# Kernel tuning notes

Measured on AMD Instinct MI355X. Metric: run time of the kernel, lower is better.

The kernel has to match this reference:

```python
import jax, jax.numpy as jnp
import numpy as np

B, T, D_MODEL, HEAD_DIM = 4, 4096, 1024, 2


def setup_inputs() -> dict:
    key = jax.random.key(0)
    kx, kq, kk, kv = jax.random.split(key, 4)
    x = jax.random.normal(kx, (B, T, D_MODEL), dtype=jnp.float32)
    # nn.Linear weights: (out_features, in_features), applied as x @ W.T
    s_qk = 1.0 / np.sqrt(D_MODEL)
    W_Q = jax.random.uniform(kq, (HEAD_DIM, D_MODEL), minval=-s_qk, maxval=s_qk, dtype=jnp.float32)
    W_K = jax.random.uniform(kk, (HEAD_DIM, D_MODEL), minval=-s_qk, maxval=s_qk, dtype=jnp.float32)
    W_V = jax.random.uniform(kv, (D_MODEL, D_MODEL), minval=-s_qk, maxval=s_qk, dtype=jnp.float32)
    # strict upper-triangular True = masked (future positions)
    causal_mask = jnp.triu(jnp.ones((T, T), dtype=bool), k=1)[None, :, :]
    return {"x": x, "W_Q": W_Q, "W_K": W_K, "W_V": W_V, "causal_mask": causal_mask}


def reference(x, W_Q, W_K, W_V, causal_mask):
    # x: (B, T, d_model)
    Q = jnp.einsum('btd,hd->bth', x, W_Q)   # (B, T, head_dim)
    K = jnp.einsum('bsd,hd->bsh', x, W_K)   # (B, S, head_dim)
    V = jnp.einsum('bsd,ed->bse', x, W_V)   # (B, S, d_model)
    scores = jnp.einsum('bth,bsh->bts', Q, K)              # (B, T, S)
    scores = jnp.where(causal_mask, -jnp.inf, scores)
    max_idx = jnp.argmax(scores, axis=-1)                  # (B, T)
    # one-hot scatter + bmm in the original == hard gather of V rows
    out = jnp.take_along_axis(V, max_idx[..., None], axis=1)  # (B, T, d_model)
    return out
```

## Files before the change

### kernel.cpp

```cpp
#include <hip/hip_runtime.h>
#include <math.h>

#define TT 4096
#define DM 1024
#define BB 4
#define BT (BB * TT)
#define SENTINEL 0x7fffffff
#define SPLIT 8


__global__ __launch_bounds__(256) void qk_kernel(const float* __restrict__ x,
                                                 const float* __restrict__ wq,
                                                 const float* __restrict__ wk,
                                                 float* __restrict__ Q,
                                                 float* __restrict__ K) {
    const int row = blockIdx.x;
    const int tid = threadIdx.x;

    const float4 xv = ((const float4*)(x + (size_t)row * DM))[tid];
    const float4 a0 = ((const float4*)(wq))[tid];
    const float4 a1 = ((const float4*)(wq + DM))[tid];
    const float4 b0 = ((const float4*)(wk))[tid];
    const float4 b1 = ((const float4*)(wk + DM))[tid];

    float s0 = xv.x * a0.x + xv.y * a0.y + xv.z * a0.z + xv.w * a0.w;
    float s1 = xv.x * a1.x + xv.y * a1.y + xv.z * a1.z + xv.w * a1.w;
    float s2 = xv.x * b0.x + xv.y * b0.y + xv.z * b0.z + xv.w * b0.w;
    float s3 = xv.x * b1.x + xv.y * b1.y + xv.z * b1.z + xv.w * b1.w;

    #pragma unroll
    for (int off = 32; off > 0; off >>= 1) {
        s0 += __shfl_down(s0, off);
        s1 += __shfl_down(s1, off);
        s2 += __shfl_down(s2, off);
        s3 += __shfl_down(s3, off);
    }
    __shared__ float red[4][4];
    const int wave = tid >> 6, lane = tid & 63;
    if (lane == 0) { red[wave][0] = s0; red[wave][1] = s1; red[wave][2] = s2; red[wave][3] = s3; }
    __syncthreads();
    if (tid == 0) {
        Q[row * 2 + 0] = red[0][0] + red[1][0] + red[2][0] + red[3][0];
        Q[row * 2 + 1] = red[0][1] + red[1][1] + red[2][1] + red[3][1];
        K[row * 2 + 0] = red[0][2] + red[1][2] + red[2][2] + red[3][2];
        K[row * 2 + 1] = red[0][3] + red[1][3] + red[2][3] + red[3][3];
    }
}

__global__ __launch_bounds__(256) void init_rep_kernel(int* __restrict__ rep,
                                                       int* __restrict__ cnt) {
    rep[blockIdx.x * 256 + threadIdx.x] = SENTINEL;
    if (blockIdx.x == 0 && threadIdx.x == 0) cnt[0] = 0;
}

__global__ __launch_bounds__(256) void argmax_kernel(const float* __restrict__ Q,
                                                     const float* __restrict__ K,
                                                     int* __restrict__ idx,
                                                     int* __restrict__ rep,
                                                     int* __restrict__ list,
                                                     int* __restrict__ cnt) {
    __shared__ float2 ks[TT];
    const int b  = blockIdx.x >> 10;
    const int tg = blockIdx.x & 1023;
    const int tid = threadIdx.x;

    const float2* kb = (const float2*)(K + (size_t)b * TT * 2);
    for (int i = tid; i < TT; i += 256) ks[i] = kb[i];
    __syncthreads();

    const int wave = tid >> 6, lane = tid & 63;
    const int t = tg * 4 + wave;
    const float2 q = ((const float2*)Q)[b * TT + t];

    float best = -INFINITY;
    int bi = 0x7fffffff;
    for (int s = lane; s <= t; s += 64) {
        const float2 kv = ks[s];
        const float sc = q.x * kv.x + q.y * kv.y;
        if (sc > best) { best = sc; bi = s; }
    }
    #pragma unroll
    for (int off = 32; off > 0; off >>= 1) {
        const float ov = __shfl_down(best, off);
        const int   oi = __shfl_down(bi, off);
        if (ov > best || (ov == best && oi < bi)) { best = ov; bi = oi; }
    }
    if (lane == 0) {
        idx[b * TT + t] = bi;
        const int old = atomicMin(&rep[b * TT + bi], t);
        if (old == SENTINEL) {
            const int p = atomicAdd(cnt, 1);
            list[p] = b * TT + bi;
        }
    }
}

__global__ __launch_bounds__(256) void vrow_kernel(const float* __restrict__ x,
                                                   const float* __restrict__ wv,
                                                   const int* __restrict__ rep,
                                                   const int* __restrict__ list,
                                                   const int* __restrict__ cnt,
                                                   float* __restrict__ out) {
    __shared__ float xs[DM];
    const int total = cnt[0] * SPLIT;
    const int tid = threadIdx.x;
    const int wave = tid >> 6, lane = tid & 63;

    for (int w = blockIdx.x; w < total; w += gridDim.x) {
        const int li = w >> 3;
        const int p  = w & (SPLIT - 1);
        const int bs = list[li];
        const int b  = bs >> 12;
        const int r  = rep[bs];

        __syncthreads();
        ((float4*)xs)[tid] = ((const float4*)(x + (size_t)bs * DM))[tid];
        __syncthreads();

        const float4 xr0 = ((const float4*)xs)[lane];
        const float4 xr1 = ((const float4*)xs)[lane + 64];
        const float4 xr2 = ((const float4*)xs)[lane + 128];
        const float4 xr3 = ((const float4*)xs)[lane + 192];

        float* orow = out + ((size_t)(b * TT + r)) * DM;
        const int ebase = p * 128 + wave * 32;

        for (int g = 0; g < 8; ++g) {
            const int e = ebase + g * 4;
            const float4* w0 = (const float4*)(wv + (size_t)(e + 0) * DM);
            const float4* w1 = (const float4*)(wv + (size_t)(e + 1) * DM);
            const float4* w2 = (const float4*)(wv + (size_t)(e + 2) * DM);
            const float4* w3 = (const float4*)(wv + (size_t)(e + 3) * DM);

            float s0 = 0.f, s1 = 0.f, s2 = 0.f, s3 = 0.f;
            #pragma unroll
            for (int k = 0; k < 4; ++k) {
                const float4 xx = (k == 0) ? xr0 : (k == 1) ? xr1 : (k == 2) ? xr2 : xr3;
                const float4 a = w0[lane + 64 * k];
                const float4 bq = w1[lane + 64 * k];
                const float4 c = w2[lane + 64 * k];
                const float4 d = w3[lane + 64 * k];
                s0 += a.x * xx.x + a.y * xx.y + a.z * xx.z + a.w * xx.w;
                s1 += bq.x * xx.x + bq.y * xx.y + bq.z * xx.z + bq.w * xx.w;
                s2 += c.x * xx.x + c.y * xx.y + c.z * xx.z + c.w * xx.w;
                s3 += d.x * xx.x + d.y * xx.y + d.z * xx.z + d.w * xx.w;
            }
            #pragma unroll
            for (int off = 32; off > 0; off >>= 1) {
                s0 += __shfl_down(s0, off);
                s1 += __shfl_down(s1, off);
                s2 += __shfl_down(s2, off);
                s3 += __shfl_down(s3, off);
            }
            if (lane == 0) *(float4*)(orow + e) = make_float4(s0, s1, s2, s3);
        }
    }
}

__global__ __launch_bounds__(256) void gather_kernel(const int* __restrict__ idx,
                                                     const int* __restrict__ rep,
                                                     float* __restrict__ out) {
    const int bt = blockIdx.x;
    const int b = bt >> 12, t = bt & (TT - 1);
    const int s = idx[bt];
    const int r = rep[b * TT + s];
    if (r == t) return;
    const float4* src = (const float4*)(out + ((size_t)(b * TT + r)) * DM);
    float4* dst = (float4*)(out + (size_t)bt * DM);
    dst[threadIdx.x] = src[threadIdx.x];
}

extern "C" void kernel_launch(void* const* d_in, const int* in_sizes, int n_in,
                              void* d_out, int out_size, void* d_ws, size_t ws_size,
                              hipStream_t stream) {
    const float* x  = (const float*)d_in[0];
    const float* wq = (const float*)d_in[1];
    const float* wk = (const float*)d_in[2];
    const float* wv = (const float*)d_in[3];
    float* out = (float*)d_out;

    char* ws = (char*)d_ws;
    float* Q    = (float*)(ws);
    float* K    = (float*)(ws + 131072);
    int*   idx  = (int*)  (ws + 262144);
    int*   rep  = (int*)  (ws + 327680);
    int*   list = (int*)  (ws + 393216);
    int*   cnt  = (int*)  (ws + 458752);

    qk_kernel<<<BT, 256, 0, stream>>>(x, wq, wk, Q, K);
    init_rep_kernel<<<BT / 256, 256, 0, stream>>>(rep, cnt);
    argmax_kernel<<<4096, 256, 0, stream>>>(Q, K, idx, rep, list, cnt);
    vrow_kernel<<<2048, 256, 0, stream>>>(x, wv, rep, list, cnt, out);
    gather_kernel<<<BT, 256, 0, stream>>>(idx, rep, out);
}
```

Before: 242.6 us.

## Fuse rep init into QK projection, trim argmax K loads, restructure V-row matvec

The QK projection now handles four rows per block, with one wave per row and the W_Q/W_K vectors staged in shared memory, and it also takes over the rep/cnt initialisation, so the separate init kernel launch is gone. The argmax kernel loads only the causal prefix of K into shared memory and unrolls its scan by four. The V-row kernel is reorganised so each wave keeps one W_V row in registers and loops over the unique selected x rows, replacing the old scheme that re-streamed four W_V rows per output chunk. The V-row change trades W_V reuse in registers for re-reading x rows across 256 slices per unique row, relying on cache hits.

```diff
diff --git a/kernel.cpp b/kernel.cpp
--- a/kernel.cpp
+++ b/kernel.cpp
@@ -6,28 +6,45 @@
 #define BB 4
 #define BT (BB * TT)
 #define SENTINEL 0x7fffffff
-#define SPLIT 8
 
+
+__device__ __forceinline__ float dot4(const float4 a, const float4 b) {
+    return a.x * b.x + a.y * b.y + a.z * b.z + a.w * b.w;
+}
 
 __global__ __launch_bounds__(256) void qk_kernel(const float* __restrict__ x,
                                                  const float* __restrict__ wq,
                                                  const float* __restrict__ wk,
                                                  float* __restrict__ Q,
-                                                 float* __restrict__ K) {
-    const int row = blockIdx.x;
+                                                 float* __restrict__ K,
+                                                 int* __restrict__ rep,
+                                                 int* __restrict__ cnt) {
+    __shared__ float4 wqs0[256], wqs1[256], wks0[256], wks1[256];
     const int tid = threadIdx.x;
+    const int row0 = blockIdx.x * 4;
 
-    const float4 xv = ((const float4*)(x + (size_t)row * DM))[tid];
-    const float4 a0 = ((const float4*)(wq))[tid];
-    const float4 a1 = ((const float4*)(wq + DM))[tid];
-    const float4 b0 = ((const float4*)(wk))[tid];
-    const float4 b1 = ((const float4*)(wk + DM))[tid];
+    wqs0[tid] = ((const float4*)(wq))[tid];
+    wqs1[tid] = ((const float4*)(wq + DM))[tid];
+    wks0[tid] = ((const float4*)(wk))[tid];
+    wks1[tid] = ((const float4*)(wk + DM))[tid];
 
-    float s0 = xv.x * a0.x + xv.y * a0.y + xv.z * a0.z + xv.w * a0.w;
-    float s1 = xv.x * a1.x + xv.y * a1.y + xv.z * a1.z + xv.w * a1.w;
-    float s2 = xv.x * b0.x + xv.y * b0.y + xv.z * b0.z + xv.w * b0.w;
-    float s3 = xv.x * b1.x + xv.y * b1.y + xv.z * b1.z + xv.w * b1.w;
+    if (tid < 4) rep[row0 + tid] = SENTINEL;
+    if (blockIdx.x == 0 && tid == 4) cnt[0] = 0;
+    __syncthreads();
 
+    const int wave = tid >> 6, lane = tid & 63;
+    const int row = row0 + wave;
+    const float4* xr = (const float4*)(x + (size_t)row * DM);
+
+    float s0 = 0.f, s1 = 0.f, s2 = 0.f, s3 = 0.f;
+    #pragma unroll
+    for (int j = 0; j < 4; ++j) {
+        const float4 xv = xr[j * 64 + lane];
+        s0 += dot4(xv, wqs0[j * 64 + lane]);
+        s1 += dot4(xv, wqs1[j * 64 + lane]);
+        s2 += dot4(xv, wks0[j * 64 + lane]);
+        s3 += dot4(xv, wks1[j * 64 + lane]);
+    }
     #pragma unroll
     for (int off = 32; off > 0; off >>= 1) {
         s0 += __shfl_down(s0, off);
@@ -35,22 +52,10 @@
         s2 += __shfl_down(s2, off);
         s3 += __shfl_down(s3, off);
     }
-    __shared__ float red[4][4];
-    const int wave = tid >> 6, lane = tid & 63;
-    if (lane == 0) { red[wave][0] = s0; red[wave][1] = s1; red[wave][2] = s2; red[wave][3] = s3; }
-    __syncthreads();
-    if (tid == 0) {
-        Q[row * 2 + 0] = red[0][0] + red[1][0] + red[2][0] + red[3][0];
-        Q[row * 2 + 1] = red[0][1] + red[1][1] + red[2][1] + red[3][1];
-        K[row * 2 + 0] = red[0][2] + red[1][2] + red[2][2] + red[3][2];
-        K[row * 2 + 1] = red[0][3] + red[1][3] + red[2][3] + red[3][3];
+    if (lane == 0) {
+        ((float2*)Q)[row] = make_float2(s0, s1);
+        ((float2*)K)[row] = make_float2(s2, s3);
     }
-}
-
-__global__ __launch_bounds__(256) void init_rep_kernel(int* __restrict__ rep,
-                                                       int* __restrict__ cnt) {
-    rep[blockIdx.x * 256 + threadIdx.x] = SENTINEL;
-    if (blockIdx.x == 0 && threadIdx.x == 0) cnt[0] = 0;
 }
 
 __global__ __launch_bounds__(256) void argmax_kernel(const float* __restrict__ Q,
@@ -63,9 +68,10 @@
     const int b  = blockIdx.x >> 10;
     const int tg = blockIdx.x & 1023;
     const int tid = threadIdx.x;
+    const int nfill = tg * 4 + 4;
 
     const float2* kb = (const float2*)(K + (size_t)b * TT * 2);
-    for (int i = tid; i < TT; i += 256) ks[i] = kb[i];
+    for (int i = tid; i < nfill; i += 256) ks[i] = kb[i];
     __syncthreads();
 
     const int wave = tid >> 6, lane = tid & 63;
@@ -74,10 +80,27 @@
 
     float best = -INFINITY;
     int bi = 0x7fffffff;
-    for (int s = lane; s <= t; s += 64) {
+    int s = lane;
+    while (s + 192 <= t) {
+        const float2 k0 = ks[s];
+        const float2 k1 = ks[s + 64];
+        const float2 k2 = ks[s + 128];
+        const float2 k3 = ks[s + 192];
+        const float c0 = q.x * k0.x + q.y * k0.y;
+        const float c1 = q.x * k1.x + q.y * k1.y;
+        const float c2 = q.x * k2.x + q.y * k2.y;
+        const float c3 = q.x * k3.x + q.y * k3.y;
+        if (c0 > best) { best = c0; bi = s; }
+        if (c1 > best) { best = c1; bi = s + 64; }
+        if (c2 > best) { best = c2; bi = s + 128; }
+        if (c3 > best) { best = c3; bi = s + 192; }
+        s += 256;
+    }
+    while (s <= t) {
         const float2 kv = ks[s];
         const float sc = q.x * kv.x + q.y * kv.y;
         if (sc > best) { best = sc; bi = s; }
+        s += 64;
     }
     #pragma unroll
     for (int off = 32; off > 0; off >>= 1) {
@@ -101,59 +124,32 @@
                                                    const int* __restrict__ list,
                                                    const int* __restrict__ cnt,
                                                    float* __restrict__ out) {
-    __shared__ float xs[DM];
-    const int total = cnt[0] * SPLIT;
-    const int tid = threadIdx.x;
-    const int wave = tid >> 6, lane = tid & 63;
+    const int tid = threadIdx.x, wave = tid >> 6, lane = tid & 63;
+    const int slice = blockIdx.x >> 3;
+    const int usub  = blockIdx.x & 7;
+    const int e = slice * 4 + wave;
 
-    for (int w = blockIdx.x; w < total; w += gridDim.x) {
-        const int li = w >> 3;
-        const int p  = w & (SPLIT - 1);
+    const float4* wrow = (const float4*)(wv + (size_t)e * DM);
+    const float4 w0 = wrow[lane];
+    const float4 w1 = wrow[lane + 64];
+    const float4 w2 = wrow[lane + 128];
+    const float4 w3 = wrow[lane + 192];
+
+    const int n = cnt[0];
+    for (int li = usub; li < n; li += 8) {
         const int bs = list[li];
         const int b  = bs >> 12;
         const int r  = rep[bs];
+        const float4* xr = (const float4*)(x + (size_t)bs * DM);
+        const float4 x0 = xr[lane];
+        const float4 x1 = xr[lane + 64];
+        const float4 x2 = xr[lane + 128];
+        const float4 x3 = xr[lane + 192];
 
-        __syncthreads();
-        ((float4*)xs)[tid] = ((const float4*)(x + (size_t)bs * DM))[tid];
-        __syncthreads();
-
-        const float4 xr0 = ((const float4*)xs)[lane];
-        const float4 xr1 = ((const float4*)xs)[lane + 64];
-        const float4 xr2 = ((const float4*)xs)[lane + 128];
-        const float4 xr3 = ((const float4*)xs)[lane + 192];
-
-        float* orow = out + ((size_t)(b * TT + r)) * DM;
-        const int ebase = p * 128 + wave * 32;
-
-        for (int g = 0; g < 8; ++g) {
-            const int e = ebase + g * 4;
-            const float4* w0 = (const float4*)(wv + (size_t)(e + 0) * DM);
-            const float4* w1 = (const float4*)(wv + (size_t)(e + 1) * DM);
-            const float4* w2 = (const float4*)(wv + (size_t)(e + 2) * DM);
-            const float4* w3 = (const float4*)(wv + (size_t)(e + 3) * DM);
-
-            float s0 = 0.f, s1 = 0.f, s2 = 0.f, s3 = 0.f;
-            #pragma unroll
-            for (int k = 0; k < 4; ++k) {
-                const float4 xx = (k == 0) ? xr0 : (k == 1) ? xr1 : (k == 2) ? xr2 : xr3;
-                const float4 a = w0[lane + 64 * k];
-                const float4 bq = w1[lane + 64 * k];
-                const float4 c = w2[lane + 64 * k];
-                const float4 d = w3[lane + 64 * k];
-                s0 += a.x * xx.x + a.y * xx.y + a.z * xx.z + a.w * xx.w;
-                s1 += bq.x * xx.x + bq.y * xx.y + bq.z * xx.z + bq.w * xx.w;
-                s2 += c.x * xx.x + c.y * xx.y + c.z * xx.z + c.w * xx.w;
-                s3 += d.x * xx.x + d.y * xx.y + d.z * xx.z + d.w * xx.w;
-            }
-            #pragma unroll
-            for (int off = 32; off > 0; off >>= 1) {
-                s0 += __shfl_down(s0, off);
-                s1 += __shfl_down(s1, off);
-                s2 += __shfl_down(s2, off);
-                s3 += __shfl_down(s3, off);
-            }
-            if (lane == 0) *(float4*)(orow + e) = make_float4(s0, s1, s2, s3);
-        }
+        float sum = dot4(w0, x0) + dot4(w1, x1) + dot4(w2, x2) + dot4(w3, x3);
+        #pragma unroll
+        for (int off = 32; off > 0; off >>= 1) sum += __shfl_down(sum, off);
+        if (lane == 0) out[((size_t)(b * TT + r)) * DM + e] = sum;
     }
 }
 
@@ -187,8 +183,7 @@
     int*   list = (int*)  (ws + 393216);
     int*   cnt  = (int*)  (ws + 458752);
 
-    qk_kernel<<<BT, 256, 0, stream>>>(x, wq, wk, Q, K);
-    init_rep_kernel<<<BT / 256, 256, 0, stream>>>(rep, cnt);
+    qk_kernel<<<BT / 4, 256, 0, stream>>>(x, wq, wk, Q, K, rep, cnt);
     argmax_kernel<<<4096, 256, 0, stream>>>(Q, K, idx, rep, list, cnt);
     vrow_kernel<<<2048, 256, 0, stream>>>(x, wv, rep, list, cnt, out);
     gather_kernel<<<BT, 256, 0, stream>>>(idx, rep, out);
```

Result: faster. 228.5 us (-5.8%).
